# Kernel tuning notes

Hardware: AMD Instinct MI355X
Metric: run time of the kernel (lower is better)

Reference implementation:

```python
import jax, jax.numpy as jnp
import numpy as np

DIM = 1024
DIM_HEAD = 64
INNER = 1024
HEADS = INNER // DIM_HEAD  # 16
QNUM = 64
MULT = 4
SCALE = DIM_HEAD ** -0.5
EPS = 1e-5


def setup_inputs() -> dict:
    key = jax.random.key(0)
    ks = jax.random.split(key, 9)
    S, B, N = 8, 128, 32
    x = jax.random.normal(ks[0], (S, B, N, DIM), dtype=jnp.float32)
    mask = jax.random.randint(ks[1], (S, B, 1), 0, 2, dtype=jnp.int32)
    q = jax.random.normal(ks[2], (QNUM, INNER), dtype=jnp.float32)
    W_kv = jax.random.normal(ks[3], (DIM, 2 * INNER), dtype=jnp.float32) * 0.02
    ln_g = jnp.ones((INNER,), dtype=jnp.float32)
    ln_b = jnp.zeros((INNER,), dtype=jnp.float32)
    W1 = jax.random.normal(ks[4], (INNER, INNER * MULT * 2), dtype=jnp.float32) * 0.02
    b1 = jnp.zeros((INNER * MULT * 2,), dtype=jnp.float32)
    W2 = jax.random.normal(ks[5], (INNER * MULT, INNER), dtype=jnp.float32) * 0.02
    b2 = jnp.zeros((INNER,), dtype=jnp.float32)
    return {"x": x, "mask": mask, "q": q, "W_kv": W_kv, "ln_g": ln_g,
            "ln_b": ln_b, "W1": W1, "b1": b1, "W2": W2, "b2": b2}


def reference(x, mask, q, W_kv, ln_g, ln_b, W1, b1, W2, b2):
    # x: (S, B, N, D) -> (S, N, B, D); attention keys run over original B axis
    x = jnp.transpose(x, (0, 2, 1, 3))
    S, N, B, _ = x.shape
    kv = x @ W_kv                                  # (S, N, B, 2*INNER)
    k, v = jnp.split(kv, 2, axis=-1)
    # split heads: (S, N, B, I) -> (S, N, H, B, Dh)
    k = k.reshape(S, N, B, HEADS, DIM_HEAD).transpose(0, 1, 3, 2, 4)
    v = v.reshape(S, N, B, HEADS, DIM_HEAD).transpose(0, 1, 3, 2, 4)
    qh = q.reshape(QNUM, HEADS, DIM_HEAD).transpose(1, 0, 2)  # (H, Q, Dh)
    sim = jnp.einsum('hqd,snhjd->snhqj', qh, k) * SCALE        # (S,N,H,Q,B)
    # mask: (S, B, J); rearrange 's i j->s j i' then [:,0,:] == mask[:, :, 0]
    m = mask[:, :, 0][:, None, None, None, :]                  # (S,1,1,1,B)
    sim = jnp.where(m == 0, jnp.float32(-1e10), sim)
    attn = jax.nn.softmax(sim, axis=-1)
    out = jnp.einsum('snhqj,snhjd->snhqd', attn, v)            # (S,N,H,Q,Dh)
    out = out.transpose(0, 1, 3, 2, 4).reshape(S, N, QNUM, INNER)
    # PreNorm(Residual(FeedForward)): y = LN(out); return FF(y) + y
    mu = jnp.mean(out, axis=-1, keepdims=True)
    var = jnp.var(out, axis=-1, keepdims=True)
    y = (out - mu) * jax.lax.rsqrt(var + EPS) * ln_g + ln_b
    u = y @ W1 + b1
    a, g = jnp.split(u, 2, axis=-1)
    ff = (a * jax.nn.gelu(g, approximate=False)) @ W2 + b2
    return ff + y
```

## Files before the change

### kernel.cpp

```cpp
#include <hip/hip_runtime.h>
#include <stdint.h>
#include <math.h>

#define SCALE  0.125f

typedef __bf16 bf16;
typedef __bf16 bf16x8 __attribute__((ext_vector_type(8)));
typedef float  f32x4  __attribute__((ext_vector_type(4)));

__device__ __forceinline__ ushort f2b(float f) {
  union { float f; uint32_t u; } v; v.f = f;
  uint32_t u = v.u;
  return (ushort)((u + 0x7fffu + ((u >> 16) & 1u)) >> 16);
}
__device__ __forceinline__ float b2f(ushort s) {
  union { uint32_t u; float f; } v; v.u = ((uint32_t)s) << 16;
  return v.f;
}
__device__ __forceinline__ void g2l16(const ushort* g, ushort* l) {
  __builtin_amdgcn_global_load_lds(
      (const __attribute__((address_space(1))) void*)g,
      (__attribute__((address_space(3))) void*)l, 16, 0, 0);
}
__device__ __forceinline__ float erf_fast(float x) {
  float ax = fabsf(x);
  float t  = __builtin_amdgcn_rcpf(1.0f + 0.3275911f * ax);
  float p  = t * (0.254829592f + t * (-0.284496736f + t * (1.421413741f +
             t * (-1.453152027f + t * 1.061405429f))));
  float e  = __expf(-ax * ax);
  float r  = 1.0f - p * e;
  return copysignf(r, x);
}

__global__ __launch_bounds__(256) void conv_x_kernel(const float* __restrict__ x,
                                                     ushort* __restrict__ xb) {
  int idx = blockIdx.x * 256 + threadIdx.x;
  int d4 = idx & 255;
  int n  = (idx >> 8) & 31;
  int b  = (idx >> 13) & 127;
  int s  = idx >> 20;
  float4 v = *(const float4*)(x + (size_t)(((s*128 + b)*32 + n) << 10) + (d4 << 2));
  ushort4 o;
  o.x = f2b(v.x); o.y = f2b(v.y); o.z = f2b(v.z); o.w = f2b(v.w);
  *(ushort4*)(xb + (size_t)(((s*32 + n)*128 + b) << 10) + (d4 << 2)) = o;
}

__global__ __launch_bounds__(256) void conv_q_kernel(const float* __restrict__ q,
                                                     ushort* __restrict__ qb) {
  int idx = blockIdx.x * 256 + threadIdx.x;
  float4 v = *(const float4*)(q + (size_t)idx * 4);
  ushort4 o;
  o.x = f2b(v.x); o.y = f2b(v.y); o.z = f2b(v.z); o.w = f2b(v.w);
  *(ushort4*)(qb + (size_t)idx * 4) = o;
}

__global__ __launch_bounds__(256) void transpose_w_kernel(const float* __restrict__ W,
                                                          ushort* __restrict__ Wt,
                                                          int K, int N, int mode) {
  __shared__ float tile[32][33];
  int rt = blockIdx.x, kt = blockIdx.y;
  int r0 = rt * 32;
  int tx = threadIdx.x & 31, ty = threadIdx.x >> 5;
  int src;
  if (mode == 1) {
    int rp = r0 + tx;
    int g6 = rp >> 6, w = rp & 63;
    src = (w < 32) ? (g6*32 + w) : (4096 + g6*32 + (w - 32));
  } else {
    src = r0 + tx;
  }
  for (int i = ty; i < 32; i += 8)
    tile[i][tx] = W[(size_t)(kt*32 + i) * N + src];
  __syncthreads();
  for (int i = ty; i < 32; i += 8)
    Wt[(size_t)(r0 + i) * K + kt*32 + tx] = f2b(tile[tx][i]);
}

template <int EPI, int K, int NCOLS>
__global__ __launch_bounds__(512, 2) void gemm256(const ushort* __restrict__ A,
                                                  const ushort* __restrict__ Bt,
                                                  float* __restrict__ outf,
                                                  ushort* __restrict__ outb,
                                                  const float* __restrict__ bias,
                                                  const float* __restrict__ resid) {
  __shared__ ushort As[2][16384];
  __shared__ ushort Bs[2][16384];
  constexpr int NT  = K / 64;
  constexpr int nBn = NCOLS / 256;

  const int nwg = (int)gridDim.x;
  const int bid = (int)blockIdx.x;
  const int wg  = (bid & 7) * (nwg >> 3) + (bid >> 3);
  const int bm = wg / nBn, bn = wg % nBn;

  const int t = threadIdx.x;
  const int wave = t >> 6, lane = t & 63;
  const int wm = wave >> 2, wn = wave & 3;
  const int c15 = lane & 15, qq = lane >> 4;
  const int swz = c15 & 7;

  const int rowc = t >> 3;
  const int kg = (t & 7) ^ (rowc & 7);
  const ushort* ag = A  + (size_t)(bm*256 + rowc) * K + kg*8;
  const ushort* bg = Bt + (size_t)(bn*256 + rowc) * K + kg*8;

  f32x4 acc[8][4] = {};

#define LDA_F(buf, mi, kh) \
  (*(const bf16x8*)(&As[buf][(wm*128 + (mi)*16 + c15)*64 + ((((kh)*4 + qq) ^ swz)*8)]))
#define LDB_F(buf, ni, kh) \
  (*(const bf16x8*)(&Bs[buf][(wn*64 + (ni)*16 + c15)*64 + ((((kh)*4 + qq) ^ swz)*8)]))
#define STG_A(c, buf, kt) \
  g2l16(ag + (size_t)(c)*64*K + (size_t)(kt)*64, &As[buf][(c)*4096 + wave*512])
#define STG_B(c, buf, kt) \
  g2l16(bg + (size_t)(c)*64*K + (size_t)(kt)*64, &Bs[buf][(c)*4096 + wave*512])

#define CFENCE asm volatile("" ::: "memory")

#define MFMA8(p, aa, ab, kh) \
  _Pragma("unroll") \
  for (int ni = 0; ni < 4; ++ni) { \
    acc[2*(p)][ni]   = __builtin_amdgcn_mfma_f32_16x16x32_bf16((aa), bfv[ni][(kh)], acc[2*(p)][ni],   0, 0, 0); \
    acc[2*(p)+1][ni] = __builtin_amdgcn_mfma_f32_16x16x32_bf16((ab), bfv[ni][(kh)], acc[2*(p)+1][ni], 0, 0, 0); \
  }

  STG_B(0, 0, 0); STG_B(1, 0, 0); STG_B(2, 0, 0); STG_B(3, 0, 0);
  STG_A(0, 0, 0); STG_A(2, 0, 0);
  CFENCE;
  STG_A(1, 0, 0); STG_A(3, 0, 0);
  asm volatile("s_waitcnt vmcnt(2)" ::: "memory");
  __builtin_amdgcn_s_barrier();
  CFENCE;

#define TILE(kt, cur) { \
    const int nx_ = (cur) ^ 1; \
    const int tn_ = ((kt) + 1 == NT) ? 0 : ((kt) + 1); \
    bf16x8 bfv[4][2]; \
     { \
      bf16x8 a00 = LDA_F(cur, 0, 0), a01 = LDA_F(cur, 0, 1); \
      bf16x8 a10 = LDA_F(cur, 1, 0), a11 = LDA_F(cur, 1, 1); \
      _Pragma("unroll") \
      for (int ni = 0; ni < 4; ++ni) { bfv[ni][0] = LDB_F(cur, ni, 0); bfv[ni][1] = LDB_F(cur, ni, 1); } \
      STG_B(0, nx_, tn_); STG_B(1, nx_, tn_); \
      __builtin_amdgcn_s_setprio(1); \
      MFMA8(0, a00, a10, 0); MFMA8(0, a01, a11, 1); \
      __builtin_amdgcn_s_setprio(0); \
      __builtin_amdgcn_s_barrier(); \
    } \
     { \
      bf16x8 a00 = LDA_F(cur, 2, 0), a01 = LDA_F(cur, 2, 1); \
      bf16x8 a10 = LDA_F(cur, 3, 0), a11 = LDA_F(cur, 3, 1); \
      STG_B(2, nx_, tn_); STG_B(3, nx_, tn_); \
      __builtin_amdgcn_s_setprio(1); \
      MFMA8(1, a00, a10, 0); MFMA8(1, a01, a11, 1); \
      __builtin_amdgcn_s_setprio(0); \
      asm volatile("s_waitcnt vmcnt(4)" ::: "memory"); \
      __builtin_amdgcn_s_barrier(); \
      CFENCE; \
    } \
     { \
      bf16x8 a00 = LDA_F(cur, 4, 0), a01 = LDA_F(cur, 4, 1); \
      bf16x8 a10 = LDA_F(cur, 5, 0), a11 = LDA_F(cur, 5, 1); \
      STG_A(0, nx_, tn_); STG_A(2, nx_, tn_); \
      __builtin_amdgcn_s_setprio(1); \
      MFMA8(2, a00, a10, 0); MFMA8(2, a01, a11, 1); \
      __builtin_amdgcn_s_setprio(0); \
      __builtin_amdgcn_s_barrier(); \
      CFENCE; \
    } \
     { \
      bf16x8 a00 = LDA_F(cur, 6, 0), a01 = LDA_F(cur, 6, 1); \
      bf16x8 a10 = LDA_F(cur, 7, 0), a11 = LDA_F(cur, 7, 1); \
      STG_A(1, nx_, tn_); STG_A(3, nx_, tn_); \
      __builtin_amdgcn_s_setprio(1); \
      MFMA8(3, a00, a10, 0); MFMA8(3, a01, a11, 1); \
      __builtin_amdgcn_s_setprio(0); \
      asm volatile("s_waitcnt lgkmcnt(0)" ::: "memory"); \
      asm volatile("s_waitcnt vmcnt(2)" ::: "memory"); \
      __builtin_amdgcn_s_barrier(); \
      CFENCE; \
    } \
  }

#pragma unroll 1
  for (int kt = 0; kt < NT; kt += 2) {
    TILE(kt, 0);
    TILE(kt + 1, 1);
  }
  asm volatile("s_waitcnt vmcnt(0)" ::: "memory");

#undef TILE
#undef MFMA8
#undef CFENCE
#undef STG_A
#undef STG_B
#undef LDA_F
#undef LDB_F

  if (EPI == 0) {
#pragma unroll
    for (int mi = 0; mi < 8; ++mi) {
      int row0 = bm*256 + wm*128 + mi*16 + qq*4;
#pragma unroll
      for (int j = 0; j < 4; ++j) {
#pragma unroll
        for (int ni = 0; ni < 4; ++ni) {
          int col = bn*256 + wn*64 + ni*16 + c15;
          outb[(size_t)(row0 + j) * NCOLS + col] = f2b(acc[mi][ni][j]);
        }
      }
    }
  } else if (EPI == 1) {
    const int g6 = bn*4 + wn;
    const int hcol0 = g6*32 + c15;
    float ba0 = bias[hcol0],        ba1 = bias[hcol0 + 16];
    float bg0 = bias[4096 + hcol0], bg1 = bias[4096 + hcol0 + 16];
#pragma unroll
    for (int mi = 0; mi < 8; ++mi) {
      int row0 = bm*256 + wm*128 + mi*16 + qq*4;
#pragma unroll
      for (int j = 0; j < 4; ++j) {
        float a0 = acc[mi][0][j] + ba0, g0 = acc[mi][2][j] + bg0;
        float a1 = acc[mi][1][j] + ba1, g1 = acc[mi][3][j] + bg1;
        float ge0 = 0.5f * g0 * (1.0f + erf_fast(g0 * 0.70710678118654752f));
        float ge1 = 0.5f * g1 * (1.0f + erf_fast(g1 * 0.70710678118654752f));
        size_t rb = (size_t)(row0 + j) * 4096;
        outb[rb + hcol0]      = f2b(a0 * ge0);
        outb[rb + hcol0 + 16] = f2b(a1 * ge1);
      }
    }
  } else {
    float bc[4];
#pragma unroll
    for (int ni = 0; ni < 4; ++ni) bc[ni] = bias[bn*256 + wn*64 + ni*16 + c15];
#pragma unroll
    for (int mi = 0; mi < 8; ++mi) {
      int row0 = bm*256 + wm*128 + mi*16 + qq*4;
#pragma unroll
      for (int j = 0; j < 4; ++j) {
#pragma unroll
        for (int ni = 0; ni < 4; ++ni) {
          int col = bn*256 + wn*64 + ni*16 + c15;
          size_t o = (size_t)(row0 + j) * NCOLS + col;
          outf[o] = acc[mi][ni][j] + bc[ni] + resid[o];
        }
      }
    }
  }
}

__global__ __launch_bounds__(256) void attn_kernel(const ushort* __restrict__ kv,
                                                   const ushort* __restrict__ qb,
                                                   const int* __restrict__ mask,
                                                   float* __restrict__ out) {
  __shared__ ushort Ks[128 * 72];
  __shared__ ushort Vt[64 * 136];
  __shared__ ushort Ps[64 * 136];
  __shared__ float  Mrow[128];

  const int bid = blockIdx.x;
  const int h = bid & 15, n = (bid >> 4) & 31, s = bid >> 9;
  const size_t kvbase = (size_t)((s*32 + n) * 128) * 2048;
  const int t = threadIdx.x, wave = t >> 6, lane = t & 63;
  const int qq = lane >> 4, r = lane & 15;

  if (t < 128) Mrow[t] = (mask[s*128 + t] == 0) ? 1.0f : 0.0f;

  for (int c = t; c < 1024; c += 256) {
    int b = c >> 3, d0 = (c & 7) * 8;
    uint4 v = *(const uint4*)(kv + kvbase + (size_t)b * 2048 + h*64 + d0);
    *(uint4*)(Ks + b*72 + d0) = v;
  }
  {
    int b = t & 127, dh = t >> 7;
    for (int jj = 0; jj < 32; jj += 8) {
      uint4 v = *(const uint4*)(kv + kvbase + (size_t)b * 2048 + 1024 + h*64 + dh*32 + jj);
      const ushort* pv = (const ushort*)&v;
#pragma unroll
      for (int u8 = 0; u8 < 8; u8++)
        Vt[(dh*32 + jj + u8)*136 + b] = pv[u8];
    }
  }
  __syncthreads();

  bf16x8 aq[2];
#pragma unroll
  for (int st = 0; st < 2; st++)
    aq[st] = *(const bf16x8*)(qb + (size_t)(wave*16 + r) * 1024 + h*64 + st*32 + qq*8);
  f32x4 sim[8];
#pragma unroll
  for (int jt = 0; jt < 8; jt++) {
    f32x4 c = {};
#pragma unroll
    for (int st = 0; st < 2; st++) {
      bf16x8 bk = *(const bf16x8*)(Ks + (jt*16 + r)*72 + st*32 + qq*8);
      c = __builtin_amdgcn_mfma_f32_16x16x32_bf16(aq[st], bk, c, 0, 0, 0);
    }
    sim[jt] = c;
  }

#pragma unroll
  for (int jt = 0; jt < 8; jt++) {
    float mflag = Mrow[jt*16 + r];
#pragma unroll
    for (int ii = 0; ii < 4; ii++) {
      float v = sim[jt][ii] * SCALE;
      sim[jt][ii] = (mflag > 0.5f) ? -1e10f : v;
    }
  }
  float mx[4] = {-3.0e38f, -3.0e38f, -3.0e38f, -3.0e38f};
#pragma unroll
  for (int jt = 0; jt < 8; jt++)
#pragma unroll
    for (int ii = 0; ii < 4; ii++) mx[ii] = fmaxf(mx[ii], sim[jt][ii]);
#pragma unroll
  for (int m = 1; m < 16; m <<= 1)
#pragma unroll
    for (int ii = 0; ii < 4; ii++) mx[ii] = fmaxf(mx[ii], __shfl_xor(mx[ii], m));
  float sm[4] = {0.f, 0.f, 0.f, 0.f};
#pragma unroll
  for (int jt = 0; jt < 8; jt++)
#pragma unroll
    for (int ii = 0; ii < 4; ii++) {
      float e = expf(sim[jt][ii] - mx[ii]);
      sim[jt][ii] = e;
      sm[ii] += e;
    }
#pragma unroll
  for (int m = 1; m < 16; m <<= 1)
#pragma unroll
    for (int ii = 0; ii < 4; ii++) sm[ii] += __shfl_xor(sm[ii], m);
#pragma unroll
  for (int ii = 0; ii < 4; ii++) sm[ii] = 1.0f / sm[ii];
#pragma unroll
  for (int jt = 0; jt < 8; jt++)
#pragma unroll
    for (int ii = 0; ii < 4; ii++)
      Ps[(wave*16 + qq*4 + ii)*136 + jt*16 + r] = f2b(sim[jt][ii] * sm[ii]);
  __syncthreads();

  f32x4 o[4] = {};
#pragma unroll
  for (int kst = 0; kst < 4; kst++) {
    bf16x8 ap = *(const bf16x8*)(Ps + (wave*16 + r)*136 + kst*32 + qq*8);
#pragma unroll
    for (int jt2 = 0; jt2 < 4; jt2++) {
      bf16x8 bv = *(const bf16x8*)(Vt + (jt2*16 + r)*136 + kst*32 + qq*8);
      o[jt2] = __builtin_amdgcn_mfma_f32_16x16x32_bf16(ap, bv, o[jt2], 0, 0, 0);
    }
  }
  const size_t orow0 = (size_t)((s*32 + n) * 64);
#pragma unroll
  for (int jt2 = 0; jt2 < 4; jt2++)
#pragma unroll
    for (int ii = 0; ii < 4; ii++) {
      int qr = wave*16 + qq*4 + ii;
      int d  = jt2*16 + r;
      out[(orow0 + qr) * 1024 + h*64 + d] = o[jt2][ii];
    }
}

__global__ __launch_bounds__(256) void ln_kernel(float* __restrict__ y,
                                                 ushort* __restrict__ yb,
                                                 const float* __restrict__ g,
                                                 const float* __restrict__ b) {
  __shared__ float r1[4], r2[4];
  const int row = blockIdx.x, t = threadIdx.x;
  const int wave = t >> 6, lane = t & 63;
  float* p = y + (size_t)row * 1024;
  float4 v = *(const float4*)(p + t*4);
  float s1 = v.x + v.y + v.z + v.w;
  float s2 = v.x*v.x + v.y*v.y + v.z*v.z + v.w*v.w;
#pragma unroll
  for (int m = 1; m < 64; m <<= 1) { s1 += __shfl_xor(s1, m); s2 += __shfl_xor(s2, m); }
  if (lane == 0) { r1[wave] = s1; r2[wave] = s2; }
  __syncthreads();
  s1 = r1[0] + r1[1] + r1[2] + r1[3];
  s2 = r2[0] + r2[1] + r2[2] + r2[3];
  float mu  = s1 * (1.0f/1024.0f);
  float var = s2 * (1.0f/1024.0f) - mu*mu;
  float inv = rsqrtf(var + 1e-5f);
  float4 gg = *(const float4*)(g + t*4);
  float4 bb = *(const float4*)(b + t*4);
  float4 o;
  o.x = (v.x - mu)*inv*gg.x + bb.x;
  o.y = (v.y - mu)*inv*gg.y + bb.y;
  o.z = (v.z - mu)*inv*gg.z + bb.z;
  o.w = (v.w - mu)*inv*gg.w + bb.w;
  *(float4*)(p + t*4) = o;
  ushort4 ob; ob.x = f2b(o.x); ob.y = f2b(o.y); ob.z = f2b(o.z); ob.w = f2b(o.w);
  *(ushort4*)(yb + (size_t)row * 1024 + t*4) = ob;
}

extern "C" void kernel_launch(void* const* d_in, const int* in_sizes, int n_in,
                              void* d_out, int out_size, void* d_ws, size_t ws_size,
                              hipStream_t stream) {
  const float* x    = (const float*)d_in[0];
  const int*   mask = (const int*)  d_in[1];
  const float* q    = (const float*)d_in[2];
  const float* Wkv  = (const float*)d_in[3];
  const float* lng  = (const float*)d_in[4];
  const float* lnb  = (const float*)d_in[5];
  const float* W1   = (const float*)d_in[6];
  const float* b1   = (const float*)d_in[7];
  const float* W2   = (const float*)d_in[8];
  const float* b2   = (const float*)d_in[9];
  float* out = (float*)d_out;
  char* ws = (char*)d_ws;

  ushort* xb   = (ushort*)(ws);
  float*  yf   = (float*) (ws);
  ushort* kvb  = (ushort*)(ws + 67108864);
  ushort* hid  = (ushort*)(ws + 67108864);
  ushort* yb   = (ushort*)(ws + 201326592);
  ushort* wkvt = (ushort*)(ws + 234881024);
  ushort* w1t  = (ushort*)(ws + 239075328);
  ushort* w2t  = (ushort*)(ws + 255852544);
  ushort* qb   = (ushort*)(ws + 264241152);

  conv_x_kernel<<<32768, 256, 0, stream>>>(x, xb);
  conv_q_kernel<<<64, 256, 0, stream>>>(q, qb);
  transpose_w_kernel<<<dim3(64, 32),  256, 0, stream>>>(Wkv, wkvt, 1024, 2048, 0);
  transpose_w_kernel<<<dim3(256, 32), 256, 0, stream>>>(W1,  w1t,  1024, 8192, 1);
  transpose_w_kernel<<<dim3(32, 128), 256, 0, stream>>>(W2,  w2t,  4096, 1024, 0);

  gemm256<0, 1024, 2048><<<1024, 512, 0, stream>>>(xb, wkvt, nullptr, kvb, nullptr, nullptr);
  attn_kernel<<<4096, 256, 0, stream>>>(kvb, qb, mask, yf);
  ln_kernel<<<16384, 256, 0, stream>>>(yf, yb, lng, lnb);
  gemm256<1, 1024, 8192><<<2048, 512, 0, stream>>>(yb, w1t, nullptr, hid, b1, nullptr);
  gemm256<2, 4096, 1024><<<256, 512, 0, stream>>>(hid, w2t, out, nullptr, b2, yf);
}
```

Baseline: 866.2 us.

## Reorder GEMM tile phases by k-half and drop two intra-tile barriers

```diff
diff --git a/kernel.cpp b/kernel.cpp
--- a/kernel.cpp
+++ b/kernel.cpp
@@ -137,43 +137,43 @@
     const int tn_ = ((kt) + 1 == NT) ? 0 : ((kt) + 1); \
     bf16x8 bfv[4][2]; \
      { \
-      bf16x8 a00 = LDA_F(cur, 0, 0), a01 = LDA_F(cur, 0, 1); \
-      bf16x8 a10 = LDA_F(cur, 1, 0), a11 = LDA_F(cur, 1, 1); \
       _Pragma("unroll") \
-      for (int ni = 0; ni < 4; ++ni) { bfv[ni][0] = LDB_F(cur, ni, 0); bfv[ni][1] = LDB_F(cur, ni, 1); } \
+      for (int ni = 0; ni < 4; ++ni) bfv[ni][0] = LDB_F(cur, ni, 0); \
+      bf16x8 a0 = LDA_F(cur, 0, 0), a1 = LDA_F(cur, 1, 0); \
+      bf16x8 a2 = LDA_F(cur, 2, 0), a3 = LDA_F(cur, 3, 0); \
       STG_B(0, nx_, tn_); STG_B(1, nx_, tn_); \
       __builtin_amdgcn_s_setprio(1); \
-      MFMA8(0, a00, a10, 0); MFMA8(0, a01, a11, 1); \
+      MFMA8(0, a0, a1, 0); MFMA8(1, a2, a3, 0); \
       __builtin_amdgcn_s_setprio(0); \
-      __builtin_amdgcn_s_barrier(); \
     } \
      { \
-      bf16x8 a00 = LDA_F(cur, 2, 0), a01 = LDA_F(cur, 2, 1); \
-      bf16x8 a10 = LDA_F(cur, 3, 0), a11 = LDA_F(cur, 3, 1); \
+      _Pragma("unroll") \
+      for (int ni = 0; ni < 4; ++ni) bfv[ni][1] = LDB_F(cur, ni, 1); \
+      bf16x8 a0 = LDA_F(cur, 0, 1), a1 = LDA_F(cur, 1, 1); \
+      bf16x8 a2 = LDA_F(cur, 2, 1), a3 = LDA_F(cur, 3, 1); \
       STG_B(2, nx_, tn_); STG_B(3, nx_, tn_); \
       __builtin_amdgcn_s_setprio(1); \
-      MFMA8(1, a00, a10, 0); MFMA8(1, a01, a11, 1); \
+      MFMA8(0, a0, a1, 1); MFMA8(1, a2, a3, 1); \
       __builtin_amdgcn_s_setprio(0); \
       asm volatile("s_waitcnt vmcnt(4)" ::: "memory"); \
       __builtin_amdgcn_s_barrier(); \
       CFENCE; \
     } \
      { \
-      bf16x8 a00 = LDA_F(cur, 4, 0), a01 = LDA_F(cur, 4, 1); \
-      bf16x8 a10 = LDA_F(cur, 5, 0), a11 = LDA_F(cur, 5, 1); \
+      bf16x8 a0 = LDA_F(cur, 4, 0), a1 = LDA_F(cur, 5, 0); \
+      bf16x8 a2 = LDA_F(cur, 6, 0), a3 = LDA_F(cur, 7, 0); \
       STG_A(0, nx_, tn_); STG_A(2, nx_, tn_); \
       __builtin_amdgcn_s_setprio(1); \
-      MFMA8(2, a00, a10, 0); MFMA8(2, a01, a11, 1); \
+      MFMA8(2, a0, a1, 0); MFMA8(3, a2, a3, 0); \
       __builtin_amdgcn_s_setprio(0); \
-      __builtin_amdgcn_s_barrier(); \
       CFENCE; \
     } \
      { \
-      bf16x8 a00 = LDA_F(cur, 6, 0), a01 = LDA_F(cur, 6, 1); \
-      bf16x8 a10 = LDA_F(cur, 7, 0), a11 = LDA_F(cur, 7, 1); \
+      bf16x8 a0 = LDA_F(cur, 4, 1), a1 = LDA_F(cur, 5, 1); \
+      bf16x8 a2 = LDA_F(cur, 6, 1), a3 = LDA_F(cur, 7, 1); \
       STG_A(1, nx_, tn_); STG_A(3, nx_, tn_); \
       __builtin_amdgcn_s_setprio(1); \
-      MFMA8(3, a00, a10, 0); MFMA8(3, a01, a11, 1); \
+      MFMA8(2, a0, a1, 1); MFMA8(3, a2, a3, 1); \
       __builtin_amdgcn_s_setprio(0); \
       asm volatile("s_waitcnt lgkmcnt(0)" ::: "memory"); \
       asm volatile("s_waitcnt vmcnt(2)" ::: "memory"); \
```

Measured after the change: 884.7 us. 2.1% more time.
